# Kernel optimization log

Hardware: AMD Instinct MI355X
Metric: run time of the kernel (lower is better)

The kernel has to match this reference:

```python
import jax, jax.numpy as jnp
import numpy as np

N = 256
DT = 1.0 / 1024.0

def _legt_discrete(n, dt):
    # HiPPO 'lmu' continuous transition
    q = np.arange(n, dtype=np.float64)
    r = (2 * q + 1)[:, None]
    j, i = np.meshgrid(q, q)
    A = np.where(i < j, -1.0, (-1.0) ** (i - j + 1)) * r   # (N, N)
    B = ((-1.0) ** q)[:, None] * r[:, 0:1]                  # (N, 1)
    B = ((-1.0) ** q[:, None] * r)                          # (N, 1)
    # bilinear (Tustin) discretization, as scipy.signal.cont2discrete
    I = np.eye(n)
    M = I - (dt / 2.0) * A
    Ad = np.linalg.solve(M, I + (dt / 2.0) * A)
    Bd = np.linalg.solve(M, dt * B).squeeze(-1)             # (N,)
    return Ad.astype(np.float32), Bd.astype(np.float32)

def setup_inputs() -> dict:
    key = jax.random.key(0)
    inputs = jax.random.normal(key, (8, 64, 1024), dtype=jnp.float32)  # (B, M, L)
    Ad, Bd = _legt_discrete(N, DT)
    return {"inputs": inputs, "A": jnp.asarray(Ad), "B": jnp.asarray(Bd)}

def reference(inputs, A, B):
    # inputs: (batch, M, L); A: (N, N); B: (N,)
    # torch: c = F.linear(c, A) + f[..., None] @ B[None]  ->  c @ A.T + outer(f, B)
    x = jnp.moveaxis(inputs, -1, 0)  # (L, batch, M)
    At = A.T
    c0 = jnp.zeros(x.shape[1:] + (A.shape[0],), dtype=inputs.dtype)  # (batch, M, N)

    def step(c, f):
        c_new = c @ At + f[..., None] * B  # (batch, M, N)
        return c_new, c_new

    _, cs = jax.lax.scan(step, c0, x)  # (L, batch, M, N)
    return cs
```

## Files before the change

kernel.cpp:

```cpp
#include <hip/hip_runtime.h>


#define LSTEPS 1024
#define CPAD 68

__global__ __launch_bounds__(1024, 4) void hippo_legt_kernel(
    const float* __restrict__ inp,
    const float* __restrict__ A,
    const float* __restrict__ Bvec,
    float* __restrict__ out)
{
    __shared__ __attribute__((aligned(16))) float cbuf[2][2][4][CPAD];
    __shared__ __attribute__((aligned(16))) float fbuf[2][LSTEPS];

    const int tid  = threadIdx.x;
    const int row  = tid >> 2;
    const int cb   = tid & 3;
    const int seq0 = blockIdx.x * 2;

    float4 a[16];
    {
        const float4* Ar = reinterpret_cast<const float4*>(A + row * 256 + cb * 64);
        #pragma unroll
        for (int k = 0; k < 16; ++k) a[k] = Ar[k];
    }
    const float bd = Bvec[row];

    if (tid < 512) {
        reinterpret_cast<float4*>(&fbuf[0][0])[tid] =
            reinterpret_cast<const float4*>(inp + (size_t)seq0 * LSTEPS)[tid];
    }
    if (tid < 2 * 4 * CPAD) {
        (&cbuf[0][0][0][0])[tid] = 0.0f;
    }
    __syncthreads();

    float* outp = out + (size_t)seq0 * 256 + row;

    auto step = [&](int cur, int nxt, int t) {
        const float f0 = fbuf[0][t];
        const float f1 = fbuf[1][t];
        const float4* c0 = reinterpret_cast<const float4*>(&cbuf[cur][0][cb][0]);
        const float4* c1 = reinterpret_cast<const float4*>(&cbuf[cur][1][cb][0]);
        float4 s0 = make_float4(0.f, 0.f, 0.f, 0.f);
        float4 s1 = make_float4(0.f, 0.f, 0.f, 0.f);
        #pragma unroll
        for (int k = 0; k < 16; ++k) {
            const float4 v0 = c0[k];
            const float4 v1 = c1[k];
            s0.x = fmaf(a[k].x, v0.x, s0.x);
            s0.y = fmaf(a[k].y, v0.y, s0.y);
            s0.z = fmaf(a[k].z, v0.z, s0.z);
            s0.w = fmaf(a[k].w, v0.w, s0.w);
            s1.x = fmaf(a[k].x, v1.x, s1.x);
            s1.y = fmaf(a[k].y, v1.y, s1.y);
            s1.z = fmaf(a[k].z, v1.z, s1.z);
            s1.w = fmaf(a[k].w, v1.w, s1.w);
        }
        float p0 = (s0.x + s0.y) + (s0.z + s0.w);
        float p1 = (s1.x + s1.y) + (s1.z + s1.w);
        p0 += __shfl_xor(p0, 1);  p0 += __shfl_xor(p0, 2);
        p1 += __shfl_xor(p1, 1);  p1 += __shfl_xor(p1, 2);
        const float cn0 = fmaf(bd, f0, p0);
        const float cn1 = fmaf(bd, f1, p1);
        if (cb == 0) {
            cbuf[nxt][0][row >> 6][row & 63] = cn0;
            cbuf[nxt][1][row >> 6][row & 63] = cn1;
            float* o = outp + (size_t)t * (512 * 256);
            o[0]   = cn0;
            o[256] = cn1;
        }
        __syncthreads();
    };

    for (int t = 0; t < LSTEPS; t += 2) {
        step(0, 1, t);
        step(1, 0, t + 1);
    }
}

extern "C" void kernel_launch(void* const* d_in, const int* in_sizes, int n_in,
                              void* d_out, int out_size, void* d_ws, size_t ws_size,
                              hipStream_t stream) {
    const float* inp = (const float*)d_in[0];
    const float* A   = (const float*)d_in[1];
    const float* B   = (const float*)d_in[2];
    float* out = (float*)d_out;
    hipLaunchKernelGGL(hippo_legt_kernel, dim3(256), dim3(1024), 0, stream,
                       inp, A, B, out);
}
```

Before: 1.771 ms.

## Retile matvec to 4 rows x 16 columns per thread with DPP reductions and packed FMA

Each thread now owns 4 output rows and a 16-column slice of A instead of 1 row and a 64-column slice. Every state vector value read from LDS is therefore reused across 4 rows, cutting LDS traffic per FMA. The math uses 2-wide float vectors so the compiler can emit packed FMA instructions. The 16-lane partial sums are reduced with DPP adds rather than shuffles, and two writer lanes store float4 results to LDS and to global memory. The cost is a longer reduction chain per row and fewer threads storing output.

```diff
diff --git a/kernel.cpp b/kernel.cpp
--- a/kernel.cpp
+++ b/kernel.cpp
@@ -2,7 +2,21 @@
 
 
 #define LSTEPS 1024
-#define CPAD 68
+#define NCH 20
+
+typedef float v2f __attribute__((ext_vector_type(2)));
+
+#define DPP_ADD(v, ctrl) \
+  ((v) + __int_as_float(__builtin_amdgcn_update_dpp( \
+       0, __float_as_int(v), (ctrl), 0xF, 0xF, false)))
+
+__device__ __forceinline__ float red16(float v) {
+  v = DPP_ADD(v, 0xB1);
+  v = DPP_ADD(v, 0x4E);
+  v = DPP_ADD(v, 0x124);
+  v = DPP_ADD(v, 0x128);
+  return v;
+}
 
 __global__ __launch_bounds__(1024, 4) void hippo_legt_kernel(
     const float* __restrict__ inp,
@@ -10,72 +24,96 @@
     const float* __restrict__ Bvec,
     float* __restrict__ out)
 {
-    __shared__ __attribute__((aligned(16))) float cbuf[2][2][4][CPAD];
+    __shared__ __attribute__((aligned(16))) float cbuf[2][2][16][NCH];
     __shared__ __attribute__((aligned(16))) float fbuf[2][LSTEPS];
 
     const int tid  = threadIdx.x;
-    const int row  = tid >> 2;
-    const int cb   = tid & 3;
+    const int rt   = tid >> 4;
+    const int ck   = tid & 15;
+    const int sq   = ck & 1;
     const int seq0 = blockIdx.x * 2;
 
-    float4 a[16];
-    {
-        const float4* Ar = reinterpret_cast<const float4*>(A + row * 256 + cb * 64);
+    v2f a[4][8];
+    #pragma unroll
+    for (int i = 0; i < 4; ++i) {
+        const float4* Ar =
+            reinterpret_cast<const float4*>(A + (size_t)(4 * rt + i) * 256 + 16 * ck);
         #pragma unroll
-        for (int k = 0; k < 16; ++k) a[k] = Ar[k];
+        for (int q = 0; q < 4; ++q) {
+            const float4 t = Ar[q];
+            a[i][2 * q]     = v2f{t.x, t.y};
+            a[i][2 * q + 1] = v2f{t.z, t.w};
+        }
     }
-    const float bd = Bvec[row];
+    const float4 bd4 = reinterpret_cast<const float4*>(Bvec)[rt];
 
     if (tid < 512) {
         reinterpret_cast<float4*>(&fbuf[0][0])[tid] =
             reinterpret_cast<const float4*>(inp + (size_t)seq0 * LSTEPS)[tid];
     }
-    if (tid < 2 * 4 * CPAD) {
-        (&cbuf[0][0][0][0])[tid] = 0.0f;
-    }
+    if (tid < 2 * 16 * NCH) (&cbuf[0][0][0][0])[tid] = 0.0f;
     __syncthreads();
 
-    float* outp = out + (size_t)seq0 * 256 + row;
+    const float4* r00 = reinterpret_cast<const float4*>(&cbuf[0][0][ck][0]);
+    const float4* r01 = reinterpret_cast<const float4*>(&cbuf[0][1][ck][0]);
+    const float4* r10 = reinterpret_cast<const float4*>(&cbuf[1][0][ck][0]);
+    const float4* r11 = reinterpret_cast<const float4*>(&cbuf[1][1][ck][0]);
+    float4* w0 = reinterpret_cast<float4*>(&cbuf[0][sq][rt >> 2][(rt & 3) * 4]);
+    float4* w1 = reinterpret_cast<float4*>(&cbuf[1][sq][rt >> 2][(rt & 3) * 4]);
+    float4* op = reinterpret_cast<float4*>(out + (size_t)(seq0 + sq) * 256 + rt * 4);
+    const bool writer = (ck < 2);
+    const size_t ostride = (size_t)512 * 256 / 4;
 
-    auto step = [&](int cur, int nxt, int t) {
-        const float f0 = fbuf[0][t];
-        const float f1 = fbuf[1][t];
-        const float4* c0 = reinterpret_cast<const float4*>(&cbuf[cur][0][cb][0]);
-        const float4* c1 = reinterpret_cast<const float4*>(&cbuf[cur][1][cb][0]);
-        float4 s0 = make_float4(0.f, 0.f, 0.f, 0.f);
-        float4 s1 = make_float4(0.f, 0.f, 0.f, 0.f);
+    auto step = [&](const float4* __restrict__ r0, const float4* __restrict__ r1,
+                    float4* w, float4* o, int t) {
+        v2f acc0[4], acc1[4];
+        {
+            const float4 u = r0[0];
+            const float4 v = r1[0];
+            const v2f ulo{u.x, u.y}, uhi{u.z, u.w};
+            const v2f vlo{v.x, v.y}, vhi{v.z, v.w};
+            #pragma unroll
+            for (int i = 0; i < 4; ++i) {
+                acc0[i] = a[i][0] * ulo;  acc0[i] += a[i][1] * uhi;
+                acc1[i] = a[i][0] * vlo;  acc1[i] += a[i][1] * vhi;
+            }
+        }
         #pragma unroll
-        for (int k = 0; k < 16; ++k) {
-            const float4 v0 = c0[k];
-            const float4 v1 = c1[k];
-            s0.x = fmaf(a[k].x, v0.x, s0.x);
-            s0.y = fmaf(a[k].y, v0.y, s0.y);
-            s0.z = fmaf(a[k].z, v0.z, s0.z);
-            s0.w = fmaf(a[k].w, v0.w, s0.w);
-            s1.x = fmaf(a[k].x, v1.x, s1.x);
-            s1.y = fmaf(a[k].y, v1.y, s1.y);
-            s1.z = fmaf(a[k].z, v1.z, s1.z);
-            s1.w = fmaf(a[k].w, v1.w, s1.w);
+        for (int q = 1; q < 4; ++q) {
+            const float4 u = r0[q];
+            const float4 v = r1[q];
+            const v2f ulo{u.x, u.y}, uhi{u.z, u.w};
+            const v2f vlo{v.x, v.y}, vhi{v.z, v.w};
+            #pragma unroll
+            for (int i = 0; i < 4; ++i) {
+                acc0[i] += a[i][2 * q]     * ulo;
+                acc0[i] += a[i][2 * q + 1] * uhi;
+                acc1[i] += a[i][2 * q]     * vlo;
+                acc1[i] += a[i][2 * q + 1] * vhi;
+            }
         }
-        float p0 = (s0.x + s0.y) + (s0.z + s0.w);
-        float p1 = (s1.x + s1.y) + (s1.z + s1.w);
-        p0 += __shfl_xor(p0, 1);  p0 += __shfl_xor(p0, 2);
-        p1 += __shfl_xor(p1, 1);  p1 += __shfl_xor(p1, 2);
-        const float cn0 = fmaf(bd, f0, p0);
-        const float cn1 = fmaf(bd, f1, p1);
-        if (cb == 0) {
-            cbuf[nxt][0][row >> 6][row & 63] = cn0;
-            cbuf[nxt][1][row >> 6][row & 63] = cn1;
-            float* o = outp + (size_t)t * (512 * 256);
-            o[0]   = cn0;
-            o[256] = cn1;
+        const float f = fbuf[sq][t];
+        float cn[4];
+        #pragma unroll
+        for (int i = 0; i < 4; ++i) {
+            float p0 = acc0[i].x + acc0[i].y;
+            float p1 = acc1[i].x + acc1[i].y;
+            p0 = red16(p0);
+            p1 = red16(p1);
+            const float ps = sq ? p1 : p0;
+            cn[i] = fmaf((&bd4.x)[i], f, ps);
+        }
+        if (writer) {
+            const float4 cv = make_float4(cn[0], cn[1], cn[2], cn[3]);
+            *w = cv;
+            *o = cv;
         }
         __syncthreads();
     };
 
     for (int t = 0; t < LSTEPS; t += 2) {
-        step(0, 1, t);
-        step(1, 0, t + 1);
+        step(r00, r01, w1, op, t);      op += ostride;
+        step(r10, r11, w0, op, t + 1);  op += ostride;
     }
 }
 
```

New measurement: 1.861 ms. 1.05x slower.
